# Optimization experiments

Hardware: AMD Instinct MI355X
Metric: run time of the kernel (lower is better)

Reference implementation:

```python
import jax, jax.numpy as jnp
import numpy as np

DIM = 768
NUM_HEADS = 12
HEAD_DIM = DIM // NUM_HEADS


def setup_inputs() -> dict:
    key = jax.random.key(0)
    k1, k2, k3 = jax.random.split(key, 3)
    B, N, C = 8, 4096, DIM
    x = jax.random.normal(k1, (B, N, C), dtype=jnp.float32)
    # torch nn.Linear weights are (out_features, in_features)
    W_qkv = jax.random.normal(k2, (3 * C, C), dtype=jnp.float32) * 0.02
    b_qkv = jnp.zeros((3 * C,), dtype=jnp.float32)
    W_proj = jax.random.normal(k3, (C, C), dtype=jnp.float32) * 0.02
    b_proj = jnp.zeros((C,), dtype=jnp.float32)
    return {"x": x, "W_qkv": W_qkv, "b_qkv": b_qkv, "W_proj": W_proj, "b_proj": b_proj}


def reference(x, W_qkv, b_qkv, W_proj, b_proj):
    B, N, C = x.shape
    H, D = NUM_HEADS, HEAD_DIM
    # qkv projection -> (3, B, H, N, D)
    qkv = (x @ W_qkv.T + b_qkv).reshape(B, N, 3, H, D).transpose(2, 0, 3, 1, 4)
    q, k, v = qkv[0], qkv[1], qkv[2]
    # feature map: elu(x) + 1 (positive kernel features)
    q = jax.nn.elu(q) + 1.0
    k = jax.nn.elu(k) + 1.0
    # kernelized linear attention: (K^T V) then Q (K^T V)
    kv = jnp.einsum('bhnd,bhnv->bhdv', k, v)          # (B,H,D,D)
    out = jnp.einsum('bhnd,bhdv->bhnv', q, kv)        # (B,H,N,D)
    k_sum = k.sum(axis=2)                             # (B,H,D)
    normalizer = jnp.einsum('bhnd,bhd->bhn', q, k_sum) + 1e-06
    out = out / normalizer[..., None]
    out = out.transpose(0, 2, 1, 3).reshape(B, N, C)
    out = out @ W_proj.T + b_proj
    return out
```

## Files before the change

kernel.cpp:

```cpp
#include <hip/hip_runtime.h>
#include <hip/hip_fp16.h>
#include <math.h>

#define NHEADS 12
#define SEQ 4096
#define BATCH 8

typedef _Float16 half8 __attribute__((ext_vector_type(8)));
typedef float floatx4 __attribute__((ext_vector_type(4)));

__global__ void zero_kernel(float* p, int n) {
  int i = blockIdx.x * 256 + threadIdx.x;
  if (i < n) p[i] = 0.f;
}

__global__ void cast_f2h(const float* __restrict__ in, __half* __restrict__ out, int n) {
  int i = (blockIdx.x * 256 + threadIdx.x) * 4;
  if (i < n) {
    float4 v = *(const float4*)&in[i];
    ushort4 o;
    o.x = __half_as_ushort(__float2half(v.x));
    o.y = __half_as_ushort(__float2half(v.y));
    o.z = __half_as_ushort(__float2half(v.z));
    o.w = __half_as_ushort(__float2half(v.w));
    *(ushort4*)&out[i] = o;
  }
}

__device__ __forceinline__ void stage_tile(const __half* __restrict__ gbase, int ldg,
                                           _Float16* lds, int t) {
#pragma unroll
  for (int it = 0; it < 2; ++it) {
    const int s  = it * 256 + t;
    const int mp = s >> 3, ps = s & 7;
    const int p  = ps ^ (mp & 7);
    const int r  = mp * 2 + (p >> 2);
    const int q  = p & 3;
    const __half* g = gbase + (size_t)r * ldg + q * 8;
    _Float16* dst = lds + (s >> 6) * 512;
    __builtin_amdgcn_global_load_lds((const __attribute__((address_space(1))) void*)g,
                                     (__attribute__((address_space(3))) void*)dst, 16, 0, 0);
  }
}
__device__ __forceinline__ void stage_blk(const __half* __restrict__ gbase, int ldg,
                                          _Float16* lds, int t) {
  const int mp = t >> 3, ps = t & 7;
  const int p  = ps ^ (mp & 7);
  const int r  = mp * 2 + (p >> 2);
  const int q  = p & 3;
  const __half* g = gbase + (size_t)r * ldg + q * 8;
  _Float16* dst = lds + (t >> 6) * 512;
  __builtin_amdgcn_global_load_lds((const __attribute__((address_space(1))) void*)g,
                                   (__attribute__((address_space(3))) void*)dst, 16, 0, 0);
}
__device__ __forceinline__ half8 read_frag(const _Float16* lds, int row, int quad) {
  const int mp = row >> 1;
  const int p  = ((row & 1) << 2) | quad;
  const int ps = p ^ (mp & 7);
  return *(const half8*)(lds + (mp * 8 + ps) * 8);
}

__device__ __forceinline__ void write_l64(_Float16* lds, int row, int col, float v) {
  lds[row * 64 + ((((col >> 3) ^ (row & 7))) << 3) + (col & 7)] = (_Float16)v;
}
__device__ __forceinline__ half8 read_l64c(const _Float16* lds, int row, int c) {
  return *(const half8*)(lds + row * 64 + ((c ^ (row & 7)) << 3));
}

__device__ __forceinline__ void barrier_raw() {
  asm volatile("s_barrier" ::: "memory");
}

__global__ __launch_bounds__(512, 2) void hgemm_kv8_kernel(
    const __half* __restrict__ A, const __half* __restrict__ W,
    const float* __restrict__ bias,
    __half* __restrict__ outK, __half* __restrict__ outV)
{
  const int K = 768;
  const int NT = 24;
  extern __shared__ __align__(16) _Float16 sh[];
  const int t    = threadIdx.x;
  const int w    = t >> 6;
  const int l    = t & 63;
  const int quad = l >> 4;
  const int mrow = l & 15;
  const int wm   = w >> 2;
  const int wn   = w & 3;

  const int bid  = blockIdx.x;
  const int xcd  = bid & 7;
  const int ii   = bid >> 3;
  const int mg   = ii / 6;
  const int jj   = ii - mg * 6;
  const int m0   = (xcd * 16 + mg) * 256;
  const int j0   = jj * 256;

  floatx4 acc[8][4];
#pragma unroll
  for (int i = 0; i < 8; ++i)
#pragma unroll
    for (int j = 0; j < 4; ++j) acc[i][j] = (floatx4){0.f, 0.f, 0.f, 0.f};

#pragma unroll
  for (int kt = 0; kt < 3; ++kt) {
    _Float16* db = sh + kt * 16384;
    const int kg = kt * 32;
    stage_blk(A + (size_t)m0 * K + kg, K, db, t);
    stage_blk(A + (size_t)(m0 + 128) * K + kg, K, db + 4096, t);
    stage_blk(W + (size_t)(768 + j0) * K + kg, K, db + 8192, t);
    stage_blk(W + (size_t)(768 + j0 + 128) * K + kg, K, db + 12288, t);
  }
  asm volatile("s_waitcnt vmcnt(8)" ::: "memory");
  barrier_raw();

#pragma unroll 4
  for (int kt = 0; kt < NT; ++kt) {
    const _Float16* bb = sh + (kt & 3) * 16384;
    const bool st = (kt + 3 < NT);
    _Float16* db = sh + ((kt + 3) & 3) * 16384;
    const int kg = (kt + 3) * 32;
    half8 af[4], bf[4];

#pragma unroll
    for (int j = 0; j < 4; ++j) {
      const int C = wn * 64 + j * 16 + mrow;
      bf[j] = read_frag(bb + 8192 + (C >> 7) * 4096, C & 127, quad);
    }
#pragma unroll
    for (int i = 0; i < 4; ++i)
      af[i] = read_frag(bb + wm * 4096, i * 16 + mrow, quad);
    if (st) {
      stage_blk(A + (size_t)m0 * K + kg, K, db, t);
      stage_blk(A + (size_t)(m0 + 128) * K + kg, K, db + 4096, t);
    }
    barrier_raw();
    __builtin_amdgcn_s_setprio(1);
#pragma unroll
    for (int i = 0; i < 4; ++i)
#pragma unroll
      for (int j = 0; j < 4; ++j)
        acc[i][j] = __builtin_amdgcn_mfma_f32_16x16x32_f16(af[i], bf[j], acc[i][j], 0, 0, 0);
    __builtin_amdgcn_s_setprio(0);

#pragma unroll
    for (int i = 0; i < 4; ++i)
      af[i] = read_frag(bb + wm * 4096, (i + 4) * 16 + mrow, quad);
    if (st) {
      stage_blk(W + (size_t)(768 + j0) * K + kg, K, db + 8192, t);
      stage_blk(W + (size_t)(768 + j0 + 128) * K + kg, K, db + 12288, t);
    }
    barrier_raw();
    __builtin_amdgcn_s_setprio(1);
#pragma unroll
    for (int i = 0; i < 4; ++i)
#pragma unroll
      for (int j = 0; j < 4; ++j)
        acc[i + 4][j] = __builtin_amdgcn_mfma_f32_16x16x32_f16(af[i], bf[j], acc[i + 4][j], 0, 0, 0);
    __builtin_amdgcn_s_setprio(0);

    if (kt < NT - 3)       asm volatile("s_waitcnt vmcnt(8)" ::: "memory");
    else if (kt == NT - 3) asm volatile("s_waitcnt vmcnt(4)" ::: "memory");
    else if (kt == NT - 2) asm volatile("s_waitcnt vmcnt(0)" ::: "memory");
    barrier_raw();
  }

  const int col0 = 768 + j0 + wn * 64;
  const int t3   = col0 / 768;
  const int h    = (col0 - t3 * 768) >> 6;
  __half* dst    = (t3 == 1) ? outK : outV;
  const int m0w  = m0 + wm * 128;
  const int b_   = m0w >> 12;
  const int n0w  = m0w & 4095;
  _Float16* scr  = sh + w * 4096;
  const size_t gbT = (size_t)(b_ * NHEADS + h) * 64 * 4096;

#pragma unroll
  for (int hf = 0; hf < 2; ++hf) {
#pragma unroll
    for (int j = 0; j < 4; ++j) {
      const int col = j * 16 + mrow;
      const float bsv = bias[col0 + col];
#pragma unroll
      for (int ii2 = 0; ii2 < 4; ++ii2)
#pragma unroll
        for (int r = 0; r < 4; ++r) {
          const int row = ii2 * 16 + quad * 4 + r;
          float val = acc[hf * 4 + ii2][j][r] + bsv;
          if (t3 == 1) val = (val > 0.f) ? (val + 1.f) : expf(val);
          write_l64(scr, col, row, val);
        }
    }
    barrier_raw();
#pragma unroll
    for (int it = 0; it < 8; ++it) {
      const int dd = it * 8 + (l >> 3);
      const int c  = l & 7;
      half8 vv = read_l64c(scr, dd, c);
      *(half8*)((_Float16*)dst + gbT + (size_t)dd * 4096 + n0w + hf * 64 + c * 8) = vv;
    }
    barrier_raw();
  }
}

__global__ __launch_bounds__(256, 3) void hgemm_proj_kernel(
    const __half* __restrict__ A, const __half* __restrict__ W,
    const float* __restrict__ bias, float* __restrict__ outF)
{
  const int K = 768;
  const int NT = 24;
  __shared__ __align__(16) _Float16 sh[3 * 8192];
  const int t    = threadIdx.x;
  const int w    = t >> 6;
  const int l    = t & 63;
  const int quad = l >> 4;
  const int mrow = l & 15;
  const int wr   = (w >> 1) * 64;
  const int wc   = (w & 1) * 64;

  const int bid  = blockIdx.x;
  const int xcd  = bid & 7;
  const int ii   = bid >> 3;
  const int mg   = ii / 6;
  const int jj   = ii - mg * 6;
  const int m0   = (xcd * 32 + mg) * 128;
  const int j0   = jj * 128;

  floatx4 acc[4][4];
#pragma unroll
  for (int i = 0; i < 4; ++i)
#pragma unroll
    for (int j = 0; j < 4; ++j) acc[i][j] = (floatx4){0.f, 0.f, 0.f, 0.f};

  stage_tile(A + (size_t)m0 * K + 0, K, sh + 0, t);
  stage_tile(W + (size_t)j0 * K + 0, K, sh + 4096, t);
  stage_tile(A + (size_t)m0 * K + 32, K, sh + 8192, t);
  stage_tile(W + (size_t)j0 * K + 32, K, sh + 12288, t);
  asm volatile("s_waitcnt vmcnt(4)" ::: "memory");
  barrier_raw();

  int cur = 0, nxt = 2;
#pragma unroll 3
  for (int kt = 0; kt < NT; ++kt) {
    const _Float16* bb = sh + cur * 8192;
    _Float16* db = sh + nxt * 8192;
    const bool st = (kt + 2 < NT);
    const int kg = (kt + 2) * 32;

    if (st) {
      stage_tile(A + (size_t)m0 * K + kg, K, db, t);
      stage_tile(W + (size_t)j0 * K + kg, K, db + 4096, t);
    }
    half8 af[4], bf[4];
#pragma unroll
    for (int i = 0; i < 4; ++i) af[i] = read_frag(bb, wr + i * 16 + mrow, quad);
#pragma unroll
    for (int j = 0; j < 4; ++j) bf[j] = read_frag(bb + 4096, wc + j * 16 + mrow, quad);
#pragma unroll
    for (int i = 0; i < 4; ++i)
#pragma unroll
      for (int j = 0; j < 4; ++j)
        acc[i][j] = __builtin_amdgcn_mfma_f32_16x16x32_f16(af[i], bf[j], acc[i][j], 0, 0, 0);

    if (kt < NT - 2)       asm volatile("s_waitcnt vmcnt(4)" ::: "memory");
    else if (kt == NT - 2) asm volatile("s_waitcnt vmcnt(0)" ::: "memory");
    barrier_raw();
    cur = (cur + 1) % 3;
    nxt = (nxt + 1) % 3;
  }

#pragma unroll
  for (int j = 0; j < 4; ++j) {
    const int col = j0 + wc + j * 16 + mrow;
    const float bsv = bias[col];
#pragma unroll
    for (int i = 0; i < 4; ++i)
#pragma unroll
      for (int r = 0; r < 4; ++r) {
        const int m = m0 + wr + i * 16 + quad * 4 + r;
        outF[(size_t)m * 768 + col] = acc[i][j][r] + bsv;
      }
  }
}

__global__ __launch_bounds__(256) void kv_mfma_kernel(
    const __half* __restrict__ kT, const __half* __restrict__ vT,
    float* __restrict__ kv, float* __restrict__ ksum)
{
  extern __shared__ float red[];
  float* ksr = red + 4 * 4096;
  const int bh = blockIdx.x;
  const int sp = blockIdx.y;
  const int t  = threadIdx.x;
  const int w  = t >> 6;
  const int l  = t & 63;
  const int quad = l >> 4;
  const int mrow = l & 15;
  const size_t base = (size_t)bh * 64 * 4096;
  const int n0 = sp * 1024 + w * 256;

  floatx4 acc[4][4];
  floatx4 ks[4];
#pragma unroll
  for (int i = 0; i < 4; ++i) {
    ks[i] = (floatx4){0.f, 0.f, 0.f, 0.f};
#pragma unroll
    for (int j = 0; j < 4; ++j) acc[i][j] = (floatx4){0.f, 0.f, 0.f, 0.f};
  }
  half8 ones;
#pragma unroll
  for (int e = 0; e < 8; ++e) ones[e] = (_Float16)1.0f;

  const __half* pk[4];
  const __half* pv[4];
#pragma unroll
  for (int i = 0; i < 4; ++i) {
    pk[i] = kT + base + (size_t)(i * 16 + mrow) * 4096 + n0 + quad * 8;
    pv[i] = vT + base + (size_t)(i * 16 + mrow) * 4096 + n0 + quad * 8;
  }

#pragma unroll
  for (int nn = 0; nn < 256; nn += 32) {
    half8 af[4], bf[4];
#pragma unroll
    for (int i = 0; i < 4; ++i) af[i] = *(const half8*)(pk[i] + nn);
#pragma unroll
    for (int j = 0; j < 4; ++j) bf[j] = *(const half8*)(pv[j] + nn);
#pragma unroll
    for (int i = 0; i < 4; ++i)
#pragma unroll
      for (int j = 0; j < 4; ++j)
        acc[i][j] = __builtin_amdgcn_mfma_f32_16x16x32_f16(af[i], bf[j], acc[i][j], 0, 0, 0);
#pragma unroll
    for (int i = 0; i < 4; ++i)
      ks[i] = __builtin_amdgcn_mfma_f32_16x16x32_f16(af[i], ones, ks[i], 0, 0, 0);
  }

  float* rw = red + w * 4096;
#pragma unroll
  for (int i = 0; i < 4; ++i)
#pragma unroll
    for (int j = 0; j < 4; ++j)
#pragma unroll
      for (int r = 0; r < 4; ++r)
        rw[(i * 16 + quad * 4 + r) * 64 + j * 16 + mrow] = acc[i][j][r];
  if (mrow == 0) {
#pragma unroll
    for (int i = 0; i < 4; ++i)
#pragma unroll
      for (int r = 0; r < 4; ++r)
        ksr[w * 64 + i * 16 + quad * 4 + r] = ks[i][r];
  }
  __syncthreads();
#pragma unroll
  for (int ii = 0; ii < 16; ++ii) {
    const int idx = ii * 256 + t;
    const float s = red[idx] + red[4096 + idx] + red[8192 + idx] + red[12288 + idx];
    atomicAdd(&kv[(size_t)bh * 4096 + idx], s);
  }
  if (t < 64)
    atomicAdd(&ksum[(size_t)bh * 64 + t], ksr[t] + ksr[64 + t] + ksr[128 + t] + ksr[192 + t]);
}

__global__ __launch_bounds__(256) void qattn_kernel(
    const __half* __restrict__ A, const __half* __restrict__ W,
    const float* __restrict__ bias,
    const float* __restrict__ kvg, const float* __restrict__ ksumg,
    __half* __restrict__ att)
{
  const int K = 768;
  __shared__ __align__(16) _Float16 sh[24576];
  _Float16* As = sh;
  _Float16* Bs = sh + 4096;
  __shared__ float norms[256];
  __shared__ float ksums[128];
  const int t    = threadIdx.x;
  const int w    = t >> 6;
  const int l    = t & 63;
  const int quad = l >> 4;
  const int mrow = l & 15;
  const int m0   = blockIdx.x * 128;
  const int j0   = blockIdx.y * 128;
  const int wr   = (w >> 1) * 64;
  const int wc   = (w & 1) * 64;
  const int b_   = m0 >> 12;
  const int h0   = j0 >> 6;

  {
    _Float16* kvT0 = sh + 16384;
#pragma unroll
    for (int ii = 0; ii < 32; ++ii) {
      const int gidx = ii * 256 + t;
      const int head = gidx >> 12;
      const int r    = gidx & 4095;
      const float val = kvg[(size_t)(b_ * NHEADS + h0 + head) * 4096 + r];
      write_l64(kvT0 + head * 4096, r & 63, r >> 6, val);
    }
    if (t < 128) ksums[t] = ksumg[(size_t)(b_ * NHEADS + h0 + (t >> 6)) * 64 + (t & 63)];
  }

  floatx4 acc[4][4];
#pragma unroll
  for (int i = 0; i < 4; ++i)
#pragma unroll
    for (int j = 0; j < 4; ++j) acc[i][j] = (floatx4){0.f, 0.f, 0.f, 0.f};

  for (int k0 = 0; k0 < K; k0 += 32) {
    __syncthreads();
    stage_tile(A + (size_t)m0 * K + k0, K, As, t);
    stage_tile(W + (size_t)j0 * K + k0, K, Bs, t);
    __syncthreads();
    half8 af[4], bf[4];
#pragma unroll
    for (int i = 0; i < 4; ++i) af[i] = read_frag(As, wr + i * 16 + mrow, quad);
#pragma unroll
    for (int j = 0; j < 4; ++j) bf[j] = read_frag(Bs, wc + j * 16 + mrow, quad);
#pragma unroll
    for (int i = 0; i < 4; ++i)
#pragma unroll
      for (int j = 0; j < 4; ++j)
        acc[i][j] = __builtin_amdgcn_mfma_f32_16x16x32_f16(af[i], bf[j], acc[i][j], 0, 0, 0);
  }

  _Float16* qtile = sh + w * 4096;
  const _Float16* kvT = sh + 16384 + (w & 1) * 4096;
  const int hh = w & 1;

  __syncthreads();
#pragma unroll
  for (int j = 0; j < 4; ++j) {
    const int col = j * 16 + mrow;
    const float bsv = bias[j0 + wc + col];
#pragma unroll
    for (int i = 0; i < 4; ++i)
#pragma unroll
      for (int r = 0; r < 4; ++r) {
        const int row = i * 16 + quad * 4 + r;
        float val = acc[i][j][r] + bsv;
        val = (val > 0.f) ? (val + 1.f) : expf(val);
        write_l64(qtile, row, col, val);
      }
  }
  __syncthreads();

  {
    float nrm = 0.f;
#pragma unroll
    for (int c = 0; c < 8; ++c) {
      half8 qv = read_l64c(qtile, l, c);
#pragma unroll
      for (int e = 0; e < 8; ++e) nrm += (float)qv[e] * ksums[hh * 64 + c * 8 + e];
    }
    norms[w * 64 + l] = 1.f / (nrm + 1e-6f);
  }

  floatx4 oacc[4][4];
#pragma unroll
  for (int i = 0; i < 4; ++i)
#pragma unroll
    for (int j = 0; j < 4; ++j) oacc[i][j] = (floatx4){0.f, 0.f, 0.f, 0.f};
#pragma unroll
  for (int ks = 0; ks < 2; ++ks) {
    half8 af[4], bf[4];
#pragma unroll
    for (int i = 0; i < 4; ++i) af[i] = read_l64c(qtile, i * 16 + mrow, ks * 4 + quad);
#pragma unroll
    for (int j = 0; j < 4; ++j) bf[j] = read_l64c(kvT, j * 16 + mrow, ks * 4 + quad);
#pragma unroll
    for (int i = 0; i < 4; ++i)
#pragma unroll
      for (int j = 0; j < 4; ++j)
        oacc[i][j] = __builtin_amdgcn_mfma_f32_16x16x32_f16(af[i], bf[j], oacc[i][j], 0, 0, 0);
  }
  __syncthreads();

#pragma unroll
  for (int i = 0; i < 4; ++i)
#pragma unroll
    for (int r = 0; r < 4; ++r) {
      const int row = i * 16 + quad * 4 + r;
      const float rn = norms[w * 64 + row];
#pragma unroll
      for (int j = 0; j < 4; ++j)
        write_l64(qtile, row, j * 16 + mrow, oacc[i][j][r] * rn);
    }
  __syncthreads();
  const int n0w = (m0 & 4095) + wr;
  const size_t abase = (size_t)(b_ * SEQ + n0w) * 768 + (h0 + hh) * 64;
#pragma unroll
  for (int it = 0; it < 8; ++it) {
    const int row = it * 8 + (l >> 3);
    const int c   = l & 7;
    half8 vv = read_l64c(qtile, row, c);
    *(half8*)((_Float16*)att + abase + (size_t)row * 768 + c * 8) = vv;
  }
}

extern "C" void kernel_launch(void* const* d_in, const int* in_sizes, int n_in,
                              void* d_out, int out_size, void* d_ws, size_t ws_size,
                              hipStream_t stream)
{
  const float* x     = (const float*)d_in[0];
  const float* Wqkv  = (const float*)d_in[1];
  const float* bqkv  = (const float*)d_in[2];
  const float* Wproj = (const float*)d_in[3];
  const float* bproj = (const float*)d_in[4];
  float* out = (float*)d_out;

  const size_t SZ = (size_t)BATCH * NHEADS * SEQ * 64;
  __half* xh  = (__half*)d_ws;
  __half* Wqh = xh + SZ;
  __half* Wph = Wqh + (size_t)2304 * 768;
  __half* R3  = Wph + (size_t)768 * 768;
  __half* R4  = R3 + SZ;
  float*  kvb = (float*)(R4 + SZ);
  float*  ksum = kvb + 96 * 64 * 64;

  static bool attr_set = false;
  if (!attr_set) {
    hipFuncSetAttribute((const void*)hgemm_kv8_kernel,
                        hipFuncAttributeMaxDynamicSharedMemorySize, 131072);
    hipFuncSetAttribute((const void*)kv_mfma_kernel,
                        hipFuncAttributeMaxDynamicSharedMemorySize, 66560);
    attr_set = true;
  }

  zero_kernel<<<1560, 256, 0, stream>>>(kvb, 96 * 64 * 64 + 96 * 64);

  cast_f2h<<<(int)(SZ / 1024), 256, 0, stream>>>(x, xh, (int)SZ);
  cast_f2h<<<(2304 * 768) / 1024, 256, 0, stream>>>(Wqkv, Wqh, 2304 * 768);
  cast_f2h<<<(768 * 768) / 1024, 256, 0, stream>>>(Wproj, Wph, 768 * 768);

  hgemm_kv8_kernel<<<768, 512, 131072, stream>>>(xh, Wqh, bqkv, R3, R4);

  kv_mfma_kernel<<<dim3(96, 4), 256, 66560, stream>>>(R3, R4, kvb, ksum);

  qattn_kernel<<<dim3(256, 6), 256, 0, stream>>>(
      xh, Wqh, bqkv, kvb, ksum, R3);

  hgemm_proj_kernel<<<1536, 256, 0, stream>>>(R3, Wph, bproj, out);
}
```

Before: 445.5 us.

## Precompute swizzled load/fragment offsets and double-buffer the Q-attention GEMM loop

Hoists the per-thread swizzle address math for the global-to-LDS loads and the LDS fragment reads out of the K loops into precomputed pointers and offsets, across all three GEMM kernels. The qattn kernel's single-buffered loop, which used two __syncthreads per K step, is replaced by a two-stage LDS double buffer. The next tile's async loads are now issued before the current tile's MFMAs. This cuts integer ALU work in the inner loops and lets global loads overlap compute in the Q kernel, at the cost of extra registers for the held offsets.

```diff
diff --git a/kernel.cpp b/kernel.cpp
--- a/kernel.cpp
+++ b/kernel.cpp
@@ -27,37 +27,15 @@
   }
 }
 
-__device__ __forceinline__ void stage_tile(const __half* __restrict__ gbase, int ldg,
-                                           _Float16* lds, int t) {
-#pragma unroll
-  for (int it = 0; it < 2; ++it) {
-    const int s  = it * 256 + t;
-    const int mp = s >> 3, ps = s & 7;
-    const int p  = ps ^ (mp & 7);
-    const int r  = mp * 2 + (p >> 2);
-    const int q  = p & 3;
-    const __half* g = gbase + (size_t)r * ldg + q * 8;
-    _Float16* dst = lds + (s >> 6) * 512;
-    __builtin_amdgcn_global_load_lds((const __attribute__((address_space(1))) void*)g,
-                                     (__attribute__((address_space(3))) void*)dst, 16, 0, 0);
-  }
-}
-__device__ __forceinline__ void stage_blk(const __half* __restrict__ gbase, int ldg,
-                                          _Float16* lds, int t) {
-  const int mp = t >> 3, ps = t & 7;
-  const int p  = ps ^ (mp & 7);
-  const int r  = mp * 2 + (p >> 2);
-  const int q  = p & 3;
-  const __half* g = gbase + (size_t)r * ldg + q * 8;
-  _Float16* dst = lds + (t >> 6) * 512;
+__device__ __forceinline__ void gld16(const __half* g, _Float16* dst) {
   __builtin_amdgcn_global_load_lds((const __attribute__((address_space(1))) void*)g,
                                    (__attribute__((address_space(3))) void*)dst, 16, 0, 0);
 }
-__device__ __forceinline__ half8 read_frag(const _Float16* lds, int row, int quad) {
+
+__device__ __forceinline__ int fragoff(int row, int quad) {
   const int mp = row >> 1;
   const int p  = ((row & 1) << 2) | quad;
-  const int ps = p ^ (mp & 7);
-  return *(const half8*)(lds + (mp * 8 + ps) * 8);
+  return (mp * 8 + (p ^ (mp & 7))) * 8;
 }
 
 __device__ __forceinline__ void write_l64(_Float16* lds, int row, int col, float v) {
@@ -95,6 +73,26 @@
   const int m0   = (xcd * 16 + mg) * 256;
   const int j0   = jj * 256;
 
+  const int mp  = t >> 3;
+  const int pp  = (t & 7) ^ (mp & 7);
+  const int rsw = mp * 2 + (pp >> 2);
+  const int qsw = (pp & 3) * 8;
+  const __half* gA0 = A + (size_t)(m0 + rsw) * K + qsw;
+  const __half* gA1 = gA0 + (size_t)128 * K;
+  const __half* gW0 = W + (size_t)(768 + j0 + rsw) * K + qsw;
+  const __half* gW1 = gW0 + (size_t)128 * K;
+  const int ld = (t >> 6) * 512;
+
+  int aoff[8], boff[4];
+#pragma unroll
+  for (int i = 0; i < 8; ++i)
+    aoff[i] = wm * 4096 + fragoff(i * 16 + mrow, quad);
+#pragma unroll
+  for (int j = 0; j < 4; ++j) {
+    const int C = wn * 64 + j * 16 + mrow;
+    boff[j] = 8192 + (C >> 7) * 4096 + fragoff(C & 127, quad);
+  }
+
   floatx4 acc[8][4];
 #pragma unroll
   for (int i = 0; i < 8; ++i)
@@ -105,10 +103,10 @@
   for (int kt = 0; kt < 3; ++kt) {
     _Float16* db = sh + kt * 16384;
     const int kg = kt * 32;
-    stage_blk(A + (size_t)m0 * K + kg, K, db, t);
-    stage_blk(A + (size_t)(m0 + 128) * K + kg, K, db + 4096, t);
-    stage_blk(W + (size_t)(768 + j0) * K + kg, K, db + 8192, t);
-    stage_blk(W + (size_t)(768 + j0 + 128) * K + kg, K, db + 12288, t);
+    gld16(gA0 + kg, db + ld);
+    gld16(gA1 + kg, db + 4096 + ld);
+    gld16(gW0 + kg, db + 8192 + ld);
+    gld16(gW1 + kg, db + 12288 + ld);
   }
   asm volatile("s_waitcnt vmcnt(8)" ::: "memory");
   barrier_raw();
@@ -122,16 +120,12 @@
     half8 af[4], bf[4];
 
 #pragma unroll
-    for (int j = 0; j < 4; ++j) {
-      const int C = wn * 64 + j * 16 + mrow;
-      bf[j] = read_frag(bb + 8192 + (C >> 7) * 4096, C & 127, quad);
-    }
-#pragma unroll
-    for (int i = 0; i < 4; ++i)
-      af[i] = read_frag(bb + wm * 4096, i * 16 + mrow, quad);
+    for (int j = 0; j < 4; ++j) bf[j] = *(const half8*)(bb + boff[j]);
+#pragma unroll
+    for (int i = 0; i < 4; ++i) af[i] = *(const half8*)(bb + aoff[i]);
     if (st) {
-      stage_blk(A + (size_t)m0 * K + kg, K, db, t);
-      stage_blk(A + (size_t)(m0 + 128) * K + kg, K, db + 4096, t);
+      gld16(gA0 + kg, db + ld);
+      gld16(gA1 + kg, db + 4096 + ld);
     }
     barrier_raw();
     __builtin_amdgcn_s_setprio(1);
@@ -143,11 +137,10 @@
     __builtin_amdgcn_s_setprio(0);
 
 #pragma unroll
-    for (int i = 0; i < 4; ++i)
-      af[i] = read_frag(bb + wm * 4096, (i + 4) * 16 + mrow, quad);
+    for (int i = 0; i < 4; ++i) af[i] = *(const half8*)(bb + aoff[i + 4]);
     if (st) {
-      stage_blk(W + (size_t)(768 + j0) * K + kg, K, db + 8192, t);
-      stage_blk(W + (size_t)(768 + j0 + 128) * K + kg, K, db + 12288, t);
+      gld16(gW0 + kg, db + 8192 + ld);
+      gld16(gW1 + kg, db + 12288 + ld);
     }
     barrier_raw();
     __builtin_amdgcn_s_setprio(1);
@@ -225,16 +218,34 @@
   const int m0   = (xcd * 32 + mg) * 128;
   const int j0   = jj * 128;
 
+  const int s1  = 256 + t;
+  const int mpa = t >> 3,  ppa = (t & 7) ^ (mpa & 7);
+  const int ra  = mpa * 2 + (ppa >> 2), qa = (ppa & 3) * 8;
+  const int mpb = s1 >> 3, ppb = (s1 & 7) ^ (mpb & 7);
+  const int rb  = mpb * 2 + (ppb >> 2), qb = (ppb & 3) * 8;
+  const int lda_ = (t >> 6) * 512;
+  const int ldb_ = (s1 >> 6) * 512;
+  const __half* gA_0 = A + (size_t)(m0 + ra) * K + qa;
+  const __half* gA_1 = A + (size_t)(m0 + rb) * K + qb;
+  const __half* gB_0 = W + (size_t)(j0 + ra) * K + qa;
+  const __half* gB_1 = W + (size_t)(j0 + rb) * K + qb;
+
+  int aoff[4], boff[4];
+#pragma unroll
+  for (int i = 0; i < 4; ++i) aoff[i] = fragoff(wr + i * 16 + mrow, quad);
+#pragma unroll
+  for (int j = 0; j < 4; ++j) boff[j] = 4096 + fragoff(wc + j * 16 + mrow, quad);
+
   floatx4 acc[4][4];
 #pragma unroll
   for (int i = 0; i < 4; ++i)
 #pragma unroll
     for (int j = 0; j < 4; ++j) acc[i][j] = (floatx4){0.f, 0.f, 0.f, 0.f};
 
-  stage_tile(A + (size_t)m0 * K + 0, K, sh + 0, t);
-  stage_tile(W + (size_t)j0 * K + 0, K, sh + 4096, t);
-  stage_tile(A + (size_t)m0 * K + 32, K, sh + 8192, t);
-  stage_tile(W + (size_t)j0 * K + 32, K, sh + 12288, t);
+  gld16(gA_0, sh + lda_);           gld16(gA_1, sh + ldb_);
+  gld16(gB_0, sh + 4096 + lda_);    gld16(gB_1, sh + 4096 + ldb_);
+  gld16(gA_0 + 32, sh + 8192 + lda_);        gld16(gA_1 + 32, sh + 8192 + ldb_);
+  gld16(gB_0 + 32, sh + 12288 + lda_);       gld16(gB_1 + 32, sh + 12288 + ldb_);
   asm volatile("s_waitcnt vmcnt(4)" ::: "memory");
   barrier_raw();
 
@@ -247,14 +258,14 @@
     const int kg = (kt + 2) * 32;
 
     if (st) {
-      stage_tile(A + (size_t)m0 * K + kg, K, db, t);
-      stage_tile(W + (size_t)j0 * K + kg, K, db + 4096, t);
+      gld16(gA_0 + kg, db + lda_);        gld16(gA_1 + kg, db + ldb_);
+      gld16(gB_0 + kg, db + 4096 + lda_); gld16(gB_1 + kg, db + 4096 + ldb_);
     }
     half8 af[4], bf[4];
 #pragma unroll
-    for (int i = 0; i < 4; ++i) af[i] = read_frag(bb, wr + i * 16 + mrow, quad);
-#pragma unroll
-    for (int j = 0; j < 4; ++j) bf[j] = read_frag(bb + 4096, wc + j * 16 + mrow, quad);
+    for (int i = 0; i < 4; ++i) af[i] = *(const half8*)(bb + aoff[i]);
+#pragma unroll
+    for (int j = 0; j < 4; ++j) bf[j] = *(const half8*)(bb + boff[j]);
 #pragma unroll
     for (int i = 0; i < 4; ++i)
 #pragma unroll
@@ -368,9 +379,8 @@
     __half* __restrict__ att)
 {
   const int K = 768;
+  const int NT = 24;
   __shared__ __align__(16) _Float16 sh[24576];
-  _Float16* As = sh;
-  _Float16* Bs = sh + 4096;
   __shared__ float norms[256];
   __shared__ float ksums[128];
   const int t    = threadIdx.x;
@@ -398,27 +408,59 @@
     if (t < 128) ksums[t] = ksumg[(size_t)(b_ * NHEADS + h0 + (t >> 6)) * 64 + (t & 63)];
   }
 
+  const int s1  = 256 + t;
+  const int mpa = t >> 3,  ppa = (t & 7) ^ (mpa & 7);
+  const int ra  = mpa * 2 + (ppa >> 2), qa = (ppa & 3) * 8;
+  const int mpb = s1 >> 3, ppb = (s1 & 7) ^ (mpb & 7);
+  const int rb  = mpb * 2 + (ppb >> 2), qb = (ppb & 3) * 8;
+  const int lda_ = (t >> 6) * 512;
+  const int ldb_ = (s1 >> 6) * 512;
+  const __half* gA_0 = A + (size_t)(m0 + ra) * K + qa;
+  const __half* gA_1 = A + (size_t)(m0 + rb) * K + qb;
+  const __half* gB_0 = W + (size_t)(j0 + ra) * K + qa;
+  const __half* gB_1 = W + (size_t)(j0 + rb) * K + qb;
+
+  int aoff[4], boff[4];
+#pragma unroll
+  for (int i = 0; i < 4; ++i) aoff[i] = fragoff(wr + i * 16 + mrow, quad);
+#pragma unroll
+  for (int j = 0; j < 4; ++j) boff[j] = 4096 + fragoff(wc + j * 16 + mrow, quad);
+
   floatx4 acc[4][4];
 #pragma unroll
   for (int i = 0; i < 4; ++i)
 #pragma unroll
     for (int j = 0; j < 4; ++j) acc[i][j] = (floatx4){0.f, 0.f, 0.f, 0.f};
 
-  for (int k0 = 0; k0 < K; k0 += 32) {
-    __syncthreads();
-    stage_tile(A + (size_t)m0 * K + k0, K, As, t);
-    stage_tile(W + (size_t)j0 * K + k0, K, Bs, t);
-    __syncthreads();
+  gld16(gA_0, sh + lda_);         gld16(gA_1, sh + ldb_);
+  gld16(gB_0, sh + 4096 + lda_);  gld16(gB_1, sh + 4096 + ldb_);
+  asm volatile("s_waitcnt vmcnt(0)" ::: "memory");
+  barrier_raw();
+
+#pragma unroll 2
+  for (int kt = 0; kt < NT; ++kt) {
+    const _Float16* bb = sh + (kt & 1) * 8192;
+    _Float16* db = sh + ((kt + 1) & 1) * 8192;
+    const bool st = (kt + 1 < NT);
+    const int kg = (kt + 1) * 32;
+
+    if (st) {
+      gld16(gA_0 + kg, db + lda_);        gld16(gA_1 + kg, db + ldb_);
+      gld16(gB_0 + kg, db + 4096 + lda_); gld16(gB_1 + kg, db + 4096 + ldb_);
+    }
     half8 af[4], bf[4];
 #pragma unroll
-    for (int i = 0; i < 4; ++i) af[i] = read_frag(As, wr + i * 16 + mrow, quad);
-#pragma unroll
-    for (int j = 0; j < 4; ++j) bf[j] = read_frag(Bs, wc + j * 16 + mrow, quad);
+    for (int i = 0; i < 4; ++i) af[i] = *(const half8*)(bb + aoff[i]);
+#pragma unroll
+    for (int j = 0; j < 4; ++j) bf[j] = *(const half8*)(bb + boff[j]);
 #pragma unroll
     for (int i = 0; i < 4; ++i)
 #pragma unroll
       for (int j = 0; j < 4; ++j)
         acc[i][j] = __builtin_amdgcn_mfma_f32_16x16x32_f16(af[i], bf[j], acc[i][j], 0, 0, 0);
+
+    if (st) asm volatile("s_waitcnt vmcnt(0)" ::: "memory");
+    barrier_raw();
   }
 
   _Float16* qtile = sh + w * 4096;
```

Result: no change. 447.2 us (+0.4%).
